# Kernel tuning notes

Hardware: AMD Instinct MI355X
Metric: run time of the kernel (lower is better)

The kernel has to match this reference:

```python
import jax, jax.numpy as jnp
import numpy as np

B, T, C, H = 4, 2048, 1024, 16
D = C // H  # head_dim = 64

def setup_inputs() -> dict:
    key = jax.random.key(0)
    ks = jax.random.split(key, 5)
    s = 0.02
    return {
        "x": jax.random.normal(ks[0], (B, T, C), dtype=jnp.float32),
        "W_attn": jax.random.normal(ks[1], (C, 3 * C), dtype=jnp.float32) * s,
        "b_attn": jnp.zeros((3 * C,), dtype=jnp.float32),
        "W_proj": jax.random.normal(ks[2], (C, C), dtype=jnp.float32) * s,
        "b_proj": jnp.zeros((C,), dtype=jnp.float32),
    }

def reference(x, W_attn, b_attn, W_proj, b_proj):
    Bx, Tx, Cx = x.shape
    qkv = x @ W_attn + b_attn                       # [B,T,3C]
    q, k, v = jnp.split(qkv, 3, axis=-1)
    def heads(t):
        return t.reshape(Bx, Tx, H, D).transpose(0, 2, 1, 3)  # [B,H,T,D]
    Q, K, V = heads(q), heads(k), heads(v)
    scale = 1.0 / np.sqrt(D).astype(np.float32)
    att = jnp.einsum('bhqd,bhkd->bhqk', Q, K) * scale        # [B,H,T,T]
    causal = jnp.tril(jnp.ones((Tx, Tx), dtype=bool))
    att = jnp.where(causal[None, None], att, -jnp.inf)
    att = jax.nn.softmax(att, axis=-1)
    y = jnp.einsum('bhqk,bhkd->bhqd', att, V)                # [B,H,T,D]
    y = y.transpose(0, 2, 1, 3).reshape(Bx, Tx, Cx)
    return y @ W_proj + b_proj
```

## Files before the change

### kernel.cpp

```cpp
#include <hip/hip_runtime.h>
#include <hip/hip_bf16.h>

#define B_ 4
#define T_ 2048
#define C_ 1024
#define H_ 16
#define D_ 64

using u16x4 = __attribute__((ext_vector_type(4))) unsigned short;
using u16x8 = __attribute__((ext_vector_type(8))) unsigned short;
using s16x8 = __attribute__((ext_vector_type(8))) short;
using f32x4v = __attribute__((ext_vector_type(4))) float;
using f32x16 = __attribute__((ext_vector_type(16))) float;

__device__ inline float bf2f(unsigned short u) {
  return __uint_as_float(((unsigned int)u) << 16);
}
__device__ inline unsigned short f2bf(float f) {
  unsigned int x = __float_as_uint(f);
  unsigned int r = (x + 0x7fffu + ((x >> 16) & 1u)) >> 16;
  return (unsigned short)r;
}
__device__ inline float fexp2(float x) {
  float r;
  asm("v_exp_f32 %0, %1" : "=v"(r) : "v"(x));
  return r;
}

__device__ inline unsigned cvtpk_bf16(float lo, float hi) {
  unsigned r;
  asm("v_cvt_pk_bf16_f32 %0, %1, %2" : "=v"(r) : "v"(lo), "v"(hi));
  return r;
}

__device__ inline s16x8 repack8(float p0, float p1, float p2, float p3,
                                float p4, float p5, float p6, float p7) {
  unsigned w0 = cvtpk_bf16(p0, p1), w1 = cvtpk_bf16(p2, p3);
  unsigned w2 = cvtpk_bf16(p4, p5), w3 = cvtpk_bf16(p6, p7);
  asm volatile("v_permlane32_swap_b32 %0, %1" : "+v"(w0), "+v"(w2));
  asm volatile("v_permlane32_swap_b32 %0, %1" : "+v"(w1), "+v"(w3));
  union { unsigned u[4]; s16x8 v; } r;
  r.u[0] = w0; r.u[1] = w1; r.u[2] = w2; r.u[3] = w3;
  return r.v;
}

__global__ __launch_bounds__(256) void cast_f32_bf16(const float* __restrict__ in,
                                                     ushort* __restrict__ out, int n4) {
  const int stride = gridDim.x * blockDim.x;
  for (int i = blockIdx.x * blockDim.x + threadIdx.x; i < n4; i += stride) {
    float4 v = ((const float4*)in)[i];
    u16x4 o = {f2bf(v.x), f2bf(v.y), f2bf(v.z), f2bf(v.w)};
    ((u16x4*)out)[i] = o;
  }
}

__global__ __launch_bounds__(256) void transpose_cast(const float* __restrict__ W,
                                                      ushort* __restrict__ Wt, int K, int N) {
  __shared__ float tile[64][65];
  const int n0 = blockIdx.x * 64, k0 = blockIdx.y * 64;
  const int tid = threadIdx.x;
  const int tr = tid >> 4, tc4 = (tid & 15) * 4;
#pragma unroll
  for (int i = 0; i < 4; ++i) {
    int r = tr + i * 16;
    float4 v = *(const float4*)&W[(size_t)(k0 + r) * N + n0 + tc4];
    tile[r][tc4 + 0] = v.x; tile[r][tc4 + 1] = v.y;
    tile[r][tc4 + 2] = v.z; tile[r][tc4 + 3] = v.w;
  }
  __syncthreads();
#pragma unroll
  for (int i = 0; i < 4; ++i) {
    int n = tr + i * 16;
    u16x4 o;
#pragma unroll
    for (int j = 0; j < 4; ++j) o[j] = f2bf(tile[tc4 + j][n]);
    *(u16x4*)&Wt[(size_t)(n0 + n) * K + k0 + tc4] = o;
  }
}

template <int BF16OUT, int NT>
__global__ __launch_bounds__(256) void gemm_bt(const ushort* __restrict__ A,
                                               const ushort* __restrict__ Bt,
                                               const float* __restrict__ bias,
                                               void* __restrict__ Cout,
                                               int M, int N, int K) {
  constexpr int BM = 128, BN = 128, BK = 64;
  __shared__ ushort Alds[2][BM * BK];
  __shared__ ushort Blds[2][BN * BK];
  const int tid = threadIdx.x;
  const int lane = tid & 63;
  const int w = tid >> 6;
  const int wr = w >> 1, wc = w & 1;
  const int nlin = blockIdx.y * gridDim.x + blockIdx.x;
  const int cpx = (gridDim.x * gridDim.y) >> 3;
  const int swzb = (nlin & 7) * cpx + (nlin >> 3);
  const int m0 = (swzb / gridDim.x) * BM;
  const int njbase = swzb % gridDim.x;

  const int ra = w * 32 + (lane >> 3);
  const int ca = ((lane & 7) * 8) ^ ((lane >> 3) << 3);
  const int swzr = (lane & 15 & 7) << 3;
  const int ko8 = (lane >> 4) * 8;
  const int l15 = lane & 15;

#define GB_STAGE(KK, BUF)                                                              \
  {                                                                                    \
    _Pragma("unroll") for (int i = 0; i < 4; ++i) {                                    \
      const ushort* ga = A + (size_t)(m0 + ra + i * 8) * K + (KK) + ca;                \
      __builtin_amdgcn_global_load_lds(                                                \
          (const __attribute__((address_space(1))) void*)ga,                           \
          (__attribute__((address_space(3))) void*)&Alds[BUF][w * 2048 + i * 512], 16, \
          0, 0);                                                                       \
      const ushort* gb = Bt + (size_t)(n0 + ra + i * 8) * K + (KK) + ca;               \
      __builtin_amdgcn_global_load_lds(                                                \
          (const __attribute__((address_space(1))) void*)gb,                           \
          (__attribute__((address_space(3))) void*)&Blds[BUF][w * 2048 + i * 512], 16, \
          0, 0);                                                                       \
    }                                                                                  \
  }

  for (int tt = 0; tt < NT; ++tt) {
    const int n0 = (njbase + tt * gridDim.x) * BN;
    f32x4v acc[4][4] = {};

    GB_STAGE(0, 0);
    asm volatile("s_waitcnt vmcnt(0)" ::: "memory");
    __builtin_amdgcn_s_barrier();
    asm volatile("" ::: "memory");

    int cur = 0;
    for (int k0 = 0; k0 < K; k0 += BK) {
      if (k0 + BK < K) GB_STAGE(k0 + BK, cur ^ 1);
#pragma unroll
      for (int ks = 0; ks < 2; ++ks) {
        s16x8 af[4], bfr[4];
#pragma unroll
        for (int m = 0; m < 4; ++m)
          af[m] = *(const s16x8*)&Alds[cur][(wr * 64 + m * 16 + l15) * BK +
                                            ((ks * 32 + ko8) ^ swzr)];
#pragma unroll
        for (int n = 0; n < 4; ++n)
          bfr[n] = *(const s16x8*)&Blds[cur][(wc * 64 + n * 16 + l15) * BK +
                                             ((ks * 32 + ko8) ^ swzr)];
#pragma unroll
        for (int m = 0; m < 4; ++m)
#pragma unroll
          for (int n = 0; n < 4; ++n)
            acc[m][n] = __builtin_amdgcn_mfma_f32_16x16x32_bf16(af[m], bfr[n], acc[m][n], 0, 0, 0);
      }
      asm volatile("s_waitcnt vmcnt(0) lgkmcnt(0)" ::: "memory");
      __builtin_amdgcn_s_barrier();
      asm volatile("" ::: "memory");
      cur ^= 1;
    }

#pragma unroll
    for (int m = 0; m < 4; ++m) {
      const int rg = m0 + wr * 64 + m * 16 + ((lane >> 4) * 4);
#pragma unroll
      for (int n = 0; n < 4; ++n) {
        const int cg = n0 + wc * 64 + n * 16 + l15;
        const float bv = bias[cg];
#pragma unroll
        for (int r2 = 0; r2 < 4; ++r2) {
          float v = acc[m][n][r2] + bv;
          if constexpr (BF16OUT)
            ((ushort*)Cout)[(size_t)(rg + r2) * N + cg] = f2bf(v);
          else
            ((float*)Cout)[(size_t)(rg + r2) * N + cg] = v;
        }
      }
    }
  }
#undef GB_STAGE
}

__global__ __launch_bounds__(256, 4) void attn_kernel(const ushort* __restrict__ qkv,
                                                      ushort* __restrict__ y) {
  constexpr int C3 = 3 * C_;
  const int n = blockIdx.x;
  const int c = n & 7;
  const int j = n >> 3;
  const int hbl = j & 7;
  const int qt = ((j >> 3) + hbl) & 15;
  const int hb = c * 8 + hbl;
  const int h = hb >> 2, b = hb & 3;
  const int tid = threadIdx.x;
  const int lane = tid & 63;
  const int w = tid >> 6;
  const int hi = lane >> 5;
  const int l31 = lane & 31;

  __shared__ __align__(16) ushort Klds[3][64 * 64];
  __shared__ __align__(16) ushort Vt[2][64 * 64];

  const int s_slot0 = (w * 2 + 0) * 1024 + lane * 16;
  const int s_slot1 = (w * 2 + 1) * 1024 + lane * 16;
  const int s_row0 = s_slot0 >> 7, s_row1 = s_slot1 >> 7;
  const int s_col0 = ((s_slot0 & 127) ^ ((s_row0 & 7) << 4)) >> 1;
  const int s_col1 = ((s_slot1 & 127) ^ ((s_row1 & 7) << 4)) >> 1;
  const ushort* kbase = qkv + (size_t)(b * T_) * C3 + C_ + h * D_;
  const ushort* vbase = qkv + (size_t)(b * T_) * C3 + 2 * C_ + h * D_;

  const int kv0 = l31 * 2;
  const int vdb = ((w << 1) | hi) * 8;

  s16x8 qf[4];
  {
    const ushort* qr = qkv + (size_t)(b * T_ + qt * 128 + w * 32 + l31) * C3 + h * D_;
#pragma unroll
    for (int ds = 0; ds < 4; ++ds) {
      s16x8 v = *(const s16x8*)(qr + ds * 16 + hi * 8);
#pragma unroll
      for (int jj = 0; jj < 8; ++jj)
        v[jj] = (short)f2bf(bf2f((unsigned short)v[jj]) * 0.18033688f);
      qf[ds] = v;
    }
  }

  const int ntile = 2 * qt + 2;
  const int nt_w = 2 * qt + 1 + (w >> 1);

  __builtin_amdgcn_global_load_lds(
      (const __attribute__((address_space(1))) void*)(kbase + (size_t)s_row0 * C3 + s_col0),
      (__attribute__((address_space(3))) void*)&Klds[0][(w * 2 + 0) * 512], 16, 0, 0);
  __builtin_amdgcn_global_load_lds(
      (const __attribute__((address_space(1))) void*)(kbase + (size_t)s_row1 * C3 + s_col1),
      (__attribute__((address_space(3))) void*)&Klds[0][(w * 2 + 1) * 512], 16, 0, 0);
  u16x8 vnA = *(const u16x8*)(vbase + (size_t)kv0 * C3 + vdb);
  u16x8 vnB = *(const u16x8*)(vbase + (size_t)(kv0 + 1) * C3 + vdb);
  if (ntile > 1) {
    __builtin_amdgcn_global_load_lds(
        (const __attribute__((address_space(1))) void*)(kbase + (size_t)(64 + s_row0) * C3 + s_col0),
        (__attribute__((address_space(3))) void*)&Klds[1][(w * 2 + 0) * 512], 16, 0, 0);
    __builtin_amdgcn_global_load_lds(
        (const __attribute__((address_space(1))) void*)(kbase + (size_t)(64 + s_row1) * C3 + s_col1),
        (__attribute__((address_space(3))) void*)&Klds[1][(w * 2 + 1) * 512], 16, 0, 0);
  }
#pragma unroll
  for (int jj = 0; jj < 8; ++jj) {
    int d = vdb + jj;
    *(unsigned*)&Vt[0][d * 64 + (kv0 ^ ((d & 7) << 3))] =
        (unsigned)vnA[jj] | ((unsigned)vnB[jj] << 16);
  }
  asm volatile("s_waitcnt lgkmcnt(0)" ::: "memory");
  __builtin_amdgcn_s_barrier();
  asm volatile("" ::: "memory");

  f32x16 yacc0 = {}, yacc1 = {};
  float lrun = 0.f;
  const int qg = qt * 128 + w * 32 + l31;

  int kcur = 0, vcur = 0;
  for (int t = 0; t < ntile; ++t) {
    const bool m1 = (t + 1 < ntile);
    const bool m2 = (t + 2 < ntile);
    if (m1) {
      const ushort* vrow = vbase + (size_t)((t + 1) * 64 + kv0) * C3;
      vnA = *(const u16x8*)(vrow + vdb);
      vnB = *(const u16x8*)(vrow + C3 + vdb);
    }
    if (m2) {
      const int kb2 = kcur >= 1 ? kcur - 1 : 2;
      __builtin_amdgcn_global_load_lds(
          (const __attribute__((address_space(1))) void*)(kbase + (size_t)((t + 2) * 64 + s_row0) * C3 + s_col0),
          (__attribute__((address_space(3))) void*)&Klds[kb2][(w * 2 + 0) * 512], 16, 0, 0);
      __builtin_amdgcn_global_load_lds(
          (const __attribute__((address_space(1))) void*)(kbase + (size_t)((t + 2) * 64 + s_row1) * C3 + s_col1),
          (__attribute__((address_space(3))) void*)&Klds[kb2][(w * 2 + 1) * 512], 16, 0, 0);
    }

    if (t < nt_w) {
      const bool diag = (t == nt_w - 1);
      const bool has_kb1 = (!diag) || ((w & 1) == 1);

      f32x16 sv0 = {}, sv1 = {};
      __builtin_amdgcn_s_setprio(1);
      {
        const int swr = (l31 & 7) << 3;
#pragma unroll
        for (int ds = 0; ds < 4; ++ds) {
          s16x8 kf = *(const s16x8*)&Klds[kcur][l31 * 64 + ((ds * 16 + hi * 8) ^ swr)];
          sv0 = __builtin_amdgcn_mfma_f32_32x32x16_bf16(kf, qf[ds], sv0, 0, 0, 0);
        }
      }
      if (has_kb1) {
        const int row = l31 + 32;
        const int swr = (row & 7) << 3;
#pragma unroll
        for (int ds = 0; ds < 4; ++ds) {
          s16x8 kf = *(const s16x8*)&Klds[kcur][row * 64 + ((ds * 16 + hi * 8) ^ swr)];
          sv1 = __builtin_amdgcn_mfma_f32_32x32x16_bf16(kf, qf[ds], sv1, 0, 0, 0);
        }
      }
      __builtin_amdgcn_s_setprio(0);

      if (diag) {
        const int kb0 = t * 64 + (w & 1) * 32 + 4 * hi;
        if ((w & 1) == 0) {
#pragma unroll
          for (int r = 0; r < 16; ++r)
            if (kb0 + (r & 3) + 8 * (r >> 2) > qg) sv0[r] = -1e30f;
        } else {
#pragma unroll
          for (int r = 0; r < 16; ++r)
            if (kb0 + (r & 3) + 8 * (r >> 2) > qg) sv1[r] = -1e30f;
        }
      }

      float l0_ = 0.f, l1_ = 0.f, l2_ = 0.f, l3_ = 0.f;
#pragma unroll
      for (int r = 0; r < 16; r += 4) {
        float p0v = fexp2(sv0[r]), p1v = fexp2(sv0[r + 1]);
        float p2v = fexp2(sv0[r + 2]), p3v = fexp2(sv0[r + 3]);
        sv0[r] = p0v; sv0[r + 1] = p1v; sv0[r + 2] = p2v; sv0[r + 3] = p3v;
        l0_ += p0v; l1_ += p1v; l2_ += p2v; l3_ += p3v;
      }
      if (has_kb1) {
#pragma unroll
        for (int r = 0; r < 16; r += 4) {
          float p0v = fexp2(sv1[r]), p1v = fexp2(sv1[r + 1]);
          float p2v = fexp2(sv1[r + 2]), p3v = fexp2(sv1[r + 3]);
          sv1[r] = p0v; sv1[r + 1] = p1v; sv1[r + 2] = p2v; sv1[r + 3] = p3v;
          l0_ += p0v; l1_ += p1v; l2_ += p2v; l3_ += p3v;
        }
      }
      float ls = (l0_ + l1_) + (l2_ + l3_);
      ls += __shfl_xor(ls, 32);
      lrun += ls;

      s16x8 pa0 = repack8(sv0[0], sv0[1], sv0[2], sv0[3], sv0[4], sv0[5], sv0[6], sv0[7]);
      s16x8 pa1 = repack8(sv0[8], sv0[9], sv0[10], sv0[11], sv0[12], sv0[13], sv0[14], sv0[15]);
      s16x8 pa2 = {}, pa3 = {};
      if (has_kb1) {
        pa2 = repack8(sv1[0], sv1[1], sv1[2], sv1[3], sv1[4], sv1[5], sv1[6], sv1[7]);
        pa3 = repack8(sv1[8], sv1[9], sv1[10], sv1[11], sv1[12], sv1[13], sv1[14], sv1[15]);
      }

      __builtin_amdgcn_s_setprio(1);
#pragma unroll
      for (int db = 0; db < 2; ++db) {
        const int d = db * 32 + l31;
        const int swz = (d & 7) << 3;
        s16x8 vf0 = *(const s16x8*)&Vt[vcur][d * 64 + ((0 + hi * 8) ^ swz)];
        s16x8 vf1 = *(const s16x8*)&Vt[vcur][d * 64 + ((16 + hi * 8) ^ swz)];
        if (db == 0) {
          yacc0 = __builtin_amdgcn_mfma_f32_32x32x16_bf16(vf0, pa0, yacc0, 0, 0, 0);
          yacc0 = __builtin_amdgcn_mfma_f32_32x32x16_bf16(vf1, pa1, yacc0, 0, 0, 0);
        } else {
          yacc1 = __builtin_amdgcn_mfma_f32_32x32x16_bf16(vf0, pa0, yacc1, 0, 0, 0);
          yacc1 = __builtin_amdgcn_mfma_f32_32x32x16_bf16(vf1, pa1, yacc1, 0, 0, 0);
        }
        if (has_kb1) {
          s16x8 vf2 = *(const s16x8*)&Vt[vcur][d * 64 + ((32 + hi * 8) ^ swz)];
          s16x8 vf3 = *(const s16x8*)&Vt[vcur][d * 64 + ((48 + hi * 8) ^ swz)];
          if (db == 0) {
            yacc0 = __builtin_amdgcn_mfma_f32_32x32x16_bf16(vf2, pa2, yacc0, 0, 0, 0);
            yacc0 = __builtin_amdgcn_mfma_f32_32x32x16_bf16(vf3, pa3, yacc0, 0, 0, 0);
          } else {
            yacc1 = __builtin_amdgcn_mfma_f32_32x32x16_bf16(vf2, pa2, yacc1, 0, 0, 0);
            yacc1 = __builtin_amdgcn_mfma_f32_32x32x16_bf16(vf3, pa3, yacc1, 0, 0, 0);
          }
        }
      }
      __builtin_amdgcn_s_setprio(0);
    }

    if (m1) {
#pragma unroll
      for (int jj = 0; jj < 8; ++jj) {
        int d = vdb + jj;
        *(unsigned*)&Vt[vcur ^ 1][d * 64 + (kv0 ^ ((d & 7) << 3))] =
            (unsigned)vnA[jj] | ((unsigned)vnB[jj] << 16);
      }
    }
    asm volatile("s_waitcnt lgkmcnt(0)" ::: "memory");
    __builtin_amdgcn_s_barrier();
    asm volatile("" ::: "memory");
    kcur = kcur == 2 ? 0 : kcur + 1;
    vcur ^= 1;
  }

  {
    const float inv = 1.f / lrun;
    yacc0 = yacc0 * inv;
    yacc1 = yacc1 * inv;
    ushort* tile = ((ushort*)Klds) + w * 2048;
    const int swq = (l31 & 7) << 3;
#pragma unroll
    for (int q4 = 0; q4 < 4; ++q4) {
      u16x4 p0, p1;
#pragma unroll
      for (int i = 0; i < 4; ++i) {
        p0[i] = f2bf(yacc0[q4 * 4 + i]);
        p1[i] = f2bf(yacc1[q4 * 4 + i]);
      }
      const int db0 = 8 * q4 + 4 * hi;
      *(u16x4*)&tile[l31 * 64 + (db0 ^ swq)] = p0;
      *(u16x4*)&tile[l31 * 64 + ((db0 + 32) ^ swq)] = p1;
    }
    const int eq = lane >> 1;
    const int ecb = (lane & 1) * 32;
    const int esz = (eq & 7) << 3;
    ushort* dst = y + (size_t)(b * T_ + qt * 128 + w * 32 + eq) * C_ + h * D_ + ecb;
#pragma unroll
    for (int cc = 0; cc < 4; ++cc) {
      u16x8 v = *(const u16x8*)&tile[eq * 64 + ((ecb + cc * 8) ^ esz)];
      *(u16x8*)(dst + cc * 8) = v;
    }
  }
}

extern "C" void kernel_launch(void* const* d_in, const int* in_sizes, int n_in,
                              void* d_out, int out_size, void* d_ws, size_t ws_size,
                              hipStream_t stream) {
  const float* x = (const float*)d_in[0];
  const float* W_attn = (const float*)d_in[1];
  const float* b_attn = (const float*)d_in[2];
  const float* W_proj = (const float*)d_in[3];
  const float* b_proj = (const float*)d_in[4];
  float* out = (float*)d_out;

  char* ws = (char*)d_ws;
  ushort* xb   = (ushort*)(ws);
  ushort* Wta  = (ushort*)(ws + (size_t)16777216);
  ushort* Wtp  = (ushort*)(ws + (size_t)23068672);
  ushort* qkvb = (ushort*)(ws + (size_t)25165824);
  ushort* yb   = (ushort*)(ws + (size_t)75497472);

  cast_f32_bf16<<<2048, 256, 0, stream>>>(x, xb, (B_ * T_ * C_) / 4);
  transpose_cast<<<dim3(48, 16), 256, 0, stream>>>(W_attn, Wta, C_, 3 * C_);
  transpose_cast<<<dim3(16, 16), 256, 0, stream>>>(W_proj, Wtp, C_, C_);
  gemm_bt<1, 3><<<dim3(8, 64), 256, 0, stream>>>(xb, Wta, b_attn, (void*)qkvb,
                                                 B_ * T_, 3 * C_, C_);
  attn_kernel<<<dim3(1024), 256, 0, stream>>>(qkvb, yb);
  gemm_bt<0, 1><<<dim3(8, 64), 256, 0, stream>>>(yb, Wtp, b_proj, (void*)out,
                                                 B_ * T_, C_, C_);
}
```

Before: 173.2 us.

## Pair causal query tiles per block to balance work and share K/V loads

Each attention block now handles two query tiles, p and 15-p, so every block does the same amount of causal work. Each K/V tile loaded into LDS is reused by both query tiles. The grid halves to 512 blocks and launch bounds drop to 2 blocks per CU, since doubled accumulators and Q fragments raise register pressure. The cost is fewer resident waves and less parallelism, which could hurt latency hiding.

```diff
diff --git a/kernel.cpp b/kernel.cpp
--- a/kernel.cpp
+++ b/kernel.cpp
@@ -175,14 +175,15 @@
 #undef GB_STAGE
 }
 
-__global__ __launch_bounds__(256, 4) void attn_kernel(const ushort* __restrict__ qkv,
+__global__ __launch_bounds__(256, 2) void attn_kernel(const ushort* __restrict__ qkv,
                                                       ushort* __restrict__ y) {
   constexpr int C3 = 3 * C_;
   const int n = blockIdx.x;
   const int c = n & 7;
   const int j = n >> 3;
   const int hbl = j & 7;
-  const int qt = ((j >> 3) + hbl) & 15;
+  const int p = j >> 3;
+  const int qtA = p, qtB = 15 - p;
   const int hb = c * 8 + hbl;
   const int h = hb >> 2, b = hb & 3;
   const int tid = threadIdx.x;
@@ -205,21 +206,29 @@
   const int kv0 = l31 * 2;
   const int vdb = ((w << 1) | hi) * 8;
 
-  s16x8 qf[4];
+  s16x8 qfA[4], qfB[4];
   {
-    const ushort* qr = qkv + (size_t)(b * T_ + qt * 128 + w * 32 + l31) * C3 + h * D_;
+    const ushort* qrA = qkv + (size_t)(b * T_ + qtA * 128 + w * 32 + l31) * C3 + h * D_;
+    const ushort* qrB = qkv + (size_t)(b * T_ + qtB * 128 + w * 32 + l31) * C3 + h * D_;
 #pragma unroll
     for (int ds = 0; ds < 4; ++ds) {
-      s16x8 v = *(const s16x8*)(qr + ds * 16 + hi * 8);
-#pragma unroll
-      for (int jj = 0; jj < 8; ++jj)
-        v[jj] = (short)f2bf(bf2f((unsigned short)v[jj]) * 0.18033688f);
-      qf[ds] = v;
-    }
-  }
-
-  const int ntile = 2 * qt + 2;
-  const int nt_w = 2 * qt + 1 + (w >> 1);
+      s16x8 va = *(const s16x8*)(qrA + ds * 16 + hi * 8);
+      s16x8 vb = *(const s16x8*)(qrB + ds * 16 + hi * 8);
+#pragma unroll
+      for (int jj = 0; jj < 8; ++jj) {
+        va[jj] = (short)f2bf(bf2f((unsigned short)va[jj]) * 0.18033688f);
+        vb[jj] = (short)f2bf(bf2f((unsigned short)vb[jj]) * 0.18033688f);
+      }
+      qfA[ds] = va;
+      qfB[ds] = vb;
+    }
+  }
+
+  const int ntile = 2 * qtB + 2;
+  const int nt_wA = 2 * qtA + 1 + (w >> 1);
+  const int nt_wB = 2 * qtB + 1 + (w >> 1);
+  const int qgA = qtA * 128 + w * 32 + l31;
+  const int qgB = qtB * 128 + w * 32 + l31;
 
   __builtin_amdgcn_global_load_lds(
       (const __attribute__((address_space(1))) void*)(kbase + (size_t)s_row0 * C3 + s_col0),
@@ -247,9 +256,93 @@
   __builtin_amdgcn_s_barrier();
   asm volatile("" ::: "memory");
 
-  f32x16 yacc0 = {}, yacc1 = {};
-  float lrun = 0.f;
-  const int qg = qt * 128 + w * 32 + l31;
+  f32x16 yaccA0 = {}, yaccA1 = {}, yaccB0 = {}, yaccB1 = {};
+  float lrunA = 0.f, lrunB = 0.f;
+
+#define ATTN_STEP(QF, Y0, Y1, LRUN, QG, NTW)                                           \
+  {                                                                                    \
+    const bool diag = (t == (NTW) - 1);                                                \
+    const bool has_kb1 = (!diag) || ((w & 1) == 1);                                    \
+    f32x16 sv0 = {}, sv1 = {};                                                         \
+    __builtin_amdgcn_s_setprio(1);                                                     \
+    {                                                                                  \
+      const int swr = (l31 & 7) << 3;                                                  \
+      _Pragma("unroll") for (int ds = 0; ds < 4; ++ds) {                               \
+        s16x8 kf = *(const s16x8*)&Klds[kcur][l31 * 64 + ((ds * 16 + hi * 8) ^ swr)];  \
+        sv0 = __builtin_amdgcn_mfma_f32_32x32x16_bf16(kf, QF[ds], sv0, 0, 0, 0);       \
+      }                                                                                \
+    }                                                                                  \
+    if (has_kb1) {                                                                     \
+      const int row = l31 + 32;                                                        \
+      const int swr = (row & 7) << 3;                                                  \
+      _Pragma("unroll") for (int ds = 0; ds < 4; ++ds) {                               \
+        s16x8 kf = *(const s16x8*)&Klds[kcur][row * 64 + ((ds * 16 + hi * 8) ^ swr)];  \
+        sv1 = __builtin_amdgcn_mfma_f32_32x32x16_bf16(kf, QF[ds], sv1, 0, 0, 0);       \
+      }                                                                                \
+    }                                                                                  \
+    __builtin_amdgcn_s_setprio(0);                                                     \
+    if (diag) {                                                                        \
+      const int kb0 = t * 64 + (w & 1) * 32 + 4 * hi;                                  \
+      if ((w & 1) == 0) {                                                              \
+        _Pragma("unroll") for (int r = 0; r < 16; ++r)                                 \
+            if (kb0 + (r & 3) + 8 * (r >> 2) > (QG)) sv0[r] = -1e30f;                  \
+      } else {                                                                         \
+        _Pragma("unroll") for (int r = 0; r < 16; ++r)                                 \
+            if (kb0 + (r & 3) + 8 * (r >> 2) > (QG)) sv1[r] = -1e30f;                  \
+      }                                                                                \
+    }                                                                                  \
+    float l0_ = 0.f, l1_ = 0.f, l2_ = 0.f, l3_ = 0.f;                                  \
+    _Pragma("unroll") for (int r = 0; r < 16; r += 4) {                                \
+      float p0v = fexp2(sv0[r]), p1v = fexp2(sv0[r + 1]);                              \
+      float p2v = fexp2(sv0[r + 2]), p3v = fexp2(sv0[r + 3]);                          \
+      sv0[r] = p0v; sv0[r + 1] = p1v; sv0[r + 2] = p2v; sv0[r + 3] = p3v;              \
+      l0_ += p0v; l1_ += p1v; l2_ += p2v; l3_ += p3v;                                  \
+    }                                                                                  \
+    if (has_kb1) {                                                                     \
+      _Pragma("unroll") for (int r = 0; r < 16; r += 4) {                              \
+        float p0v = fexp2(sv1[r]), p1v = fexp2(sv1[r + 1]);                            \
+        float p2v = fexp2(sv1[r + 2]), p3v = fexp2(sv1[r + 3]);                        \
+        sv1[r] = p0v; sv1[r + 1] = p1v; sv1[r + 2] = p2v; sv1[r + 3] = p3v;            \
+        l0_ += p0v; l1_ += p1v; l2_ += p2v; l3_ += p3v;                                \
+      }                                                                                \
+    }                                                                                  \
+    float ls = (l0_ + l1_) + (l2_ + l3_);                                              \
+    ls += __shfl_xor(ls, 32);                                                          \
+    LRUN += ls;                                                                        \
+    s16x8 pa0 = repack8(sv0[0], sv0[1], sv0[2], sv0[3], sv0[4], sv0[5], sv0[6], sv0[7]);  \
+    s16x8 pa1 = repack8(sv0[8], sv0[9], sv0[10], sv0[11], sv0[12], sv0[13], sv0[14], sv0[15]); \
+    s16x8 pa2 = {}, pa3 = {};                                                          \
+    if (has_kb1) {                                                                     \
+      pa2 = repack8(sv1[0], sv1[1], sv1[2], sv1[3], sv1[4], sv1[5], sv1[6], sv1[7]);   \
+      pa3 = repack8(sv1[8], sv1[9], sv1[10], sv1[11], sv1[12], sv1[13], sv1[14], sv1[15]); \
+    }                                                                                  \
+    __builtin_amdgcn_s_setprio(1);                                                     \
+    _Pragma("unroll") for (int db = 0; db < 2; ++db) {                                 \
+      const int d = db * 32 + l31;                                                     \
+      const int swz = (d & 7) << 3;                                                    \
+      s16x8 vf0 = *(const s16x8*)&Vt[vcur][d * 64 + ((0 + hi * 8) ^ swz)];             \
+      s16x8 vf1 = *(const s16x8*)&Vt[vcur][d * 64 + ((16 + hi * 8) ^ swz)];            \
+      if (db == 0) {                                                                   \
+        Y0 = __builtin_amdgcn_mfma_f32_32x32x16_bf16(vf0, pa0, Y0, 0, 0, 0);           \
+        Y0 = __builtin_amdgcn_mfma_f32_32x32x16_bf16(vf1, pa1, Y0, 0, 0, 0);           \
+      } else {                                                                         \
+        Y1 = __builtin_amdgcn_mfma_f32_32x32x16_bf16(vf0, pa0, Y1, 0, 0, 0);           \
+        Y1 = __builtin_amdgcn_mfma_f32_32x32x16_bf16(vf1, pa1, Y1, 0, 0, 0);           \
+      }                                                                                \
+      if (has_kb1) {                                                                   \
+        s16x8 vf2 = *(const s16x8*)&Vt[vcur][d * 64 + ((32 + hi * 8) ^ swz)];          \
+        s16x8 vf3 = *(const s16x8*)&Vt[vcur][d * 64 + ((48 + hi * 8) ^ swz)];          \
+        if (db == 0) {                                                                 \
+          Y0 = __builtin_amdgcn_mfma_f32_32x32x16_bf16(vf2, pa2, Y0, 0, 0, 0);         \
+          Y0 = __builtin_amdgcn_mfma_f32_32x32x16_bf16(vf3, pa3, Y0, 0, 0, 0);         \
+        } else {                                                                       \
+          Y1 = __builtin_amdgcn_mfma_f32_32x32x16_bf16(vf2, pa2, Y1, 0, 0, 0);         \
+          Y1 = __builtin_amdgcn_mfma_f32_32x32x16_bf16(vf3, pa3, Y1, 0, 0, 0);         \
+        }                                                                              \
+      }                                                                                \
+    }                                                                                  \
+    __builtin_amdgcn_s_setprio(0);                                                     \
+  }
 
   int kcur = 0, vcur = 0;
   for (int t = 0; t < ntile; ++t) {
@@ -270,101 +363,8 @@
           (__attribute__((address_space(3))) void*)&Klds[kb2][(w * 2 + 1) * 512], 16, 0, 0);
     }
 
-    if (t < nt_w) {
-      const bool diag = (t == nt_w - 1);
-      const bool has_kb1 = (!diag) || ((w & 1) == 1);
-
-      f32x16 sv0 = {}, sv1 = {};
-      __builtin_amdgcn_s_setprio(1);
-      {
-        const int swr = (l31 & 7) << 3;
-#pragma unroll
-        for (int ds = 0; ds < 4; ++ds) {
-          s16x8 kf = *(const s16x8*)&Klds[kcur][l31 * 64 + ((ds * 16 + hi * 8) ^ swr)];
-          sv0 = __builtin_amdgcn_mfma_f32_32x32x16_bf16(kf, qf[ds], sv0, 0, 0, 0);
-        }
-      }
-      if (has_kb1) {
-        const int row = l31 + 32;
-        const int swr = (row & 7) << 3;
-#pragma unroll
-        for (int ds = 0; ds < 4; ++ds) {
-          s16x8 kf = *(const s16x8*)&Klds[kcur][row * 64 + ((ds * 16 + hi * 8) ^ swr)];
-          sv1 = __builtin_amdgcn_mfma_f32_32x32x16_bf16(kf, qf[ds], sv1, 0, 0, 0);
-        }
-      }
-      __builtin_amdgcn_s_setprio(0);
-
-      if (diag) {
-        const int kb0 = t * 64 + (w & 1) * 32 + 4 * hi;
-        if ((w & 1) == 0) {
-#pragma unroll
-          for (int r = 0; r < 16; ++r)
-            if (kb0 + (r & 3) + 8 * (r >> 2) > qg) sv0[r] = -1e30f;
-        } else {
-#pragma unroll
-          for (int r = 0; r < 16; ++r)
-            if (kb0 + (r & 3) + 8 * (r >> 2) > qg) sv1[r] = -1e30f;
-        }
-      }
-
-      float l0_ = 0.f, l1_ = 0.f, l2_ = 0.f, l3_ = 0.f;
-#pragma unroll
-      for (int r = 0; r < 16; r += 4) {
-        float p0v = fexp2(sv0[r]), p1v = fexp2(sv0[r + 1]);
-        float p2v = fexp2(sv0[r + 2]), p3v = fexp2(sv0[r + 3]);
-        sv0[r] = p0v; sv0[r + 1] = p1v; sv0[r + 2] = p2v; sv0[r + 3] = p3v;
-        l0_ += p0v; l1_ += p1v; l2_ += p2v; l3_ += p3v;
-      }
-      if (has_kb1) {
-#pragma unroll
-        for (int r = 0; r < 16; r += 4) {
-          float p0v = fexp2(sv1[r]), p1v = fexp2(sv1[r + 1]);
-          float p2v = fexp2(sv1[r + 2]), p3v = fexp2(sv1[r + 3]);
-          sv1[r] = p0v; sv1[r + 1] = p1v; sv1[r + 2] = p2v; sv1[r + 3] = p3v;
-          l0_ += p0v; l1_ += p1v; l2_ += p2v; l3_ += p3v;
-        }
-      }
-      float ls = (l0_ + l1_) + (l2_ + l3_);
-      ls += __shfl_xor(ls, 32);
-      lrun += ls;
-
-      s16x8 pa0 = repack8(sv0[0], sv0[1], sv0[2], sv0[3], sv0[4], sv0[5], sv0[6], sv0[7]);
-      s16x8 pa1 = repack8(sv0[8], sv0[9], sv0[10], sv0[11], sv0[12], sv0[13], sv0[14], sv0[15]);
-      s16x8 pa2 = {}, pa3 = {};
-      if (has_kb1) {
-        pa2 = repack8(sv1[0], sv1[1], sv1[2], sv1[3], sv1[4], sv1[5], sv1[6], sv1[7]);
-        pa3 = repack8(sv1[8], sv1[9], sv1[10], sv1[11], sv1[12], sv1[13], sv1[14], sv1[15]);
-      }
-
-      __builtin_amdgcn_s_setprio(1);
-#pragma unroll
-      for (int db = 0; db < 2; ++db) {
-        const int d = db * 32 + l31;
-        const int swz = (d & 7) << 3;
-        s16x8 vf0 = *(const s16x8*)&Vt[vcur][d * 64 + ((0 + hi * 8) ^ swz)];
-        s16x8 vf1 = *(const s16x8*)&Vt[vcur][d * 64 + ((16 + hi * 8) ^ swz)];
-        if (db == 0) {
-          yacc0 = __builtin_amdgcn_mfma_f32_32x32x16_bf16(vf0, pa0, yacc0, 0, 0, 0);
-          yacc0 = __builtin_amdgcn_mfma_f32_32x32x16_bf16(vf1, pa1, yacc0, 0, 0, 0);
-        } else {
-          yacc1 = __builtin_amdgcn_mfma_f32_32x32x16_bf16(vf0, pa0, yacc1, 0, 0, 0);
-          yacc1 = __builtin_amdgcn_mfma_f32_32x32x16_bf16(vf1, pa1, yacc1, 0, 0, 0);
-        }
-        if (has_kb1) {
-          s16x8 vf2 = *(const s16x8*)&Vt[vcur][d * 64 + ((32 + hi * 8) ^ swz)];
-          s16x8 vf3 = *(const s16x8*)&Vt[vcur][d * 64 + ((48 + hi * 8) ^ swz)];
-          if (db == 0) {
-            yacc0 = __builtin_amdgcn_mfma_f32_32x32x16_bf16(vf2, pa2, yacc0, 0, 0, 0);
-            yacc0 = __builtin_amdgcn_mfma_f32_32x32x16_bf16(vf3, pa3, yacc0, 0, 0, 0);
-          } else {
-            yacc1 = __builtin_amdgcn_mfma_f32_32x32x16_bf16(vf2, pa2, yacc1, 0, 0, 0);
-            yacc1 = __builtin_amdgcn_mfma_f32_32x32x16_bf16(vf3, pa3, yacc1, 0, 0, 0);
-          }
-        }
-      }
-      __builtin_amdgcn_s_setprio(0);
-    }
+    if (t < nt_wB) ATTN_STEP(qfB, yaccB0, yaccB1, lrunB, qgB, nt_wB);
+    if (t < nt_wA) ATTN_STEP(qfA, yaccA0, yaccA1, lrunA, qgA, nt_wA);
 
     if (m1) {
 #pragma unroll
@@ -380,33 +380,42 @@
     kcur = kcur == 2 ? 0 : kcur + 1;
     vcur ^= 1;
   }
+#undef ATTN_STEP
 
   {
-    const float inv = 1.f / lrun;
-    yacc0 = yacc0 * inv;
-    yacc1 = yacc1 * inv;
-    ushort* tile = ((ushort*)Klds) + w * 2048;
     const int swq = (l31 & 7) << 3;
-#pragma unroll
-    for (int q4 = 0; q4 < 4; ++q4) {
-      u16x4 p0, p1;
-#pragma unroll
-      for (int i = 0; i < 4; ++i) {
-        p0[i] = f2bf(yacc0[q4 * 4 + i]);
-        p1[i] = f2bf(yacc1[q4 * 4 + i]);
-      }
-      const int db0 = 8 * q4 + 4 * hi;
-      *(u16x4*)&tile[l31 * 64 + (db0 ^ swq)] = p0;
-      *(u16x4*)&tile[l31 * 64 + ((db0 + 32) ^ swq)] = p1;
-    }
     const int eq = lane >> 1;
     const int ecb = (lane & 1) * 32;
     const int esz = (eq & 7) << 3;
-    ushort* dst = y + (size_t)(b * T_ + qt * 128 + w * 32 + eq) * C_ + h * D_ + ecb;
+    ushort* tileA = ((ushort*)Klds) + w * 2048;
+    ushort* tileB = ((ushort*)Vt) + w * 2048;
+    const float invA = 1.f / lrunA, invB = 1.f / lrunB;
+    yaccA0 = yaccA0 * invA; yaccA1 = yaccA1 * invA;
+    yaccB0 = yaccB0 * invB; yaccB1 = yaccB1 * invB;
+#pragma unroll
+    for (int q4 = 0; q4 < 4; ++q4) {
+      u16x4 a0, a1, b0, b1;
+#pragma unroll
+      for (int i = 0; i < 4; ++i) {
+        a0[i] = f2bf(yaccA0[q4 * 4 + i]);
+        a1[i] = f2bf(yaccA1[q4 * 4 + i]);
+        b0[i] = f2bf(yaccB0[q4 * 4 + i]);
+        b1[i] = f2bf(yaccB1[q4 * 4 + i]);
+      }
+      const int db0 = 8 * q4 + 4 * hi;
+      *(u16x4*)&tileA[l31 * 64 + (db0 ^ swq)] = a0;
+      *(u16x4*)&tileA[l31 * 64 + ((db0 + 32) ^ swq)] = a1;
+      *(u16x4*)&tileB[l31 * 64 + (db0 ^ swq)] = b0;
+      *(u16x4*)&tileB[l31 * 64 + ((db0 + 32) ^ swq)] = b1;
+    }
+    ushort* dstA = y + (size_t)(b * T_ + qtA * 128 + w * 32 + eq) * C_ + h * D_ + ecb;
+    ushort* dstB = y + (size_t)(b * T_ + qtB * 128 + w * 32 + eq) * C_ + h * D_ + ecb;
 #pragma unroll
     for (int cc = 0; cc < 4; ++cc) {
-      u16x8 v = *(const u16x8*)&tile[eq * 64 + ((ecb + cc * 8) ^ esz)];
-      *(u16x8*)(dst + cc * 8) = v;
+      u16x8 va = *(const u16x8*)&tileA[eq * 64 + ((ecb + cc * 8) ^ esz)];
+      u16x8 vb = *(const u16x8*)&tileB[eq * 64 + ((ecb + cc * 8) ^ esz)];
+      *(u16x8*)(dstA + cc * 8) = va;
+      *(u16x8*)(dstB + cc * 8) = vb;
     }
   }
 }
@@ -433,7 +442,7 @@
   transpose_cast<<<dim3(16, 16), 256, 0, stream>>>(W_proj, Wtp, C_, C_);
   gemm_bt<1, 3><<<dim3(8, 64), 256, 0, stream>>>(xb, Wta, b_attn, (void*)qkvb,
                                                  B_ * T_, 3 * C_, C_);
-  attn_kernel<<<dim3(1024), 256, 0, stream>>>(qkvb, yb);
+  attn_kernel<<<dim3(512), 256, 0, stream>>>(qkvb, yb);
   gemm_bt<0, 1><<<dim3(8, 64), 256, 0, stream>>>(yb, Wtp, b_proj, (void*)out,
                                                  B_ * T_, C_, C_);
 }
```

After: 165.8 us. 1.04x faster.

## Enlarge attention blocks to 256 query rows sharing K/V tiles across 8 waves

Applied to the files above, without the earlier changes.

Each attention workgroup now covers 256 query rows with 8 waves instead of 128 rows with 4 waves. Each K/V tile staged in shared memory is therefore reused by twice as many waves, which halves global K/V traffic per query. Query blocks are assigned in a folded order (0..3 then 7..4) to balance causal work, and the staging indices are reworked so each thread loads one 16-byte chunk. In exchange, V is written to LDS with 16-bit scalar stores instead of packed 32-bit stores. The launch bound of 512 threads with a minimum of 4 blocks per CU may squeeze registers and cause spills, and there are half as many blocks with more idle waves near the causal diagonal.

```diff
diff --git a/kernel.cpp b/kernel.cpp
--- a/kernel.cpp
+++ b/kernel.cpp
@@ -175,14 +175,15 @@
 #undef GB_STAGE
 }
 
-__global__ __launch_bounds__(256, 4) void attn_kernel(const ushort* __restrict__ qkv,
+__global__ __launch_bounds__(512, 4) void attn_kernel(const ushort* __restrict__ qkv,
                                                       ushort* __restrict__ y) {
   constexpr int C3 = 3 * C_;
   const int n = blockIdx.x;
   const int c = n & 7;
   const int j = n >> 3;
   const int hbl = j & 7;
-  const int qt = ((j >> 3) + hbl) & 15;
+  const int u = j >> 3;
+  const int qb = (u < 4) ? u : 11 - u;
   const int hb = c * 8 + hbl;
   const int h = hb >> 2, b = hb & 3;
   const int tid = threadIdx.x;
@@ -191,23 +192,19 @@
   const int hi = lane >> 5;
   const int l31 = lane & 31;
 
-  __shared__ __align__(16) ushort Klds[3][64 * 64];
-  __shared__ __align__(16) ushort Vt[2][64 * 64];
-
-  const int s_slot0 = (w * 2 + 0) * 1024 + lane * 16;
-  const int s_slot1 = (w * 2 + 1) * 1024 + lane * 16;
-  const int s_row0 = s_slot0 >> 7, s_row1 = s_slot1 >> 7;
-  const int s_col0 = ((s_slot0 & 127) ^ ((s_row0 & 7) << 4)) >> 1;
-  const int s_col1 = ((s_slot1 & 127) ^ ((s_row1 & 7) << 4)) >> 1;
+  __shared__ __align__(16) ushort SH[5 * 4096];
+
+  const int s_row = tid >> 3;
+  const int s_col = (((tid & 7) * 16) ^ ((s_row & 7) << 4)) >> 1;
   const ushort* kbase = qkv + (size_t)(b * T_) * C3 + C_ + h * D_;
   const ushort* vbase = qkv + (size_t)(b * T_) * C3 + 2 * C_ + h * D_;
 
-  const int kv0 = l31 * 2;
-  const int vdb = ((w << 1) | hi) * 8;
+  const int kvr = tid >> 3;
+  const int vdb = (tid & 7) * 8;
 
   s16x8 qf[4];
   {
-    const ushort* qr = qkv + (size_t)(b * T_ + qt * 128 + w * 32 + l31) * C3 + h * D_;
+    const ushort* qr = qkv + (size_t)(b * T_ + qb * 256 + w * 32 + l31) * C3 + h * D_;
 #pragma unroll
     for (int ds = 0; ds < 4; ++ds) {
       s16x8 v = *(const s16x8*)(qr + ds * 16 + hi * 8);
@@ -218,30 +215,23 @@
     }
   }
 
-  const int ntile = 2 * qt + 2;
-  const int nt_w = 2 * qt + 1 + (w >> 1);
+  const int ntile = 4 * qb + 4;
+  const int nt_w = 4 * qb + (w >> 1) + 1;
+  const int qg = qb * 256 + w * 32 + l31;
 
   __builtin_amdgcn_global_load_lds(
-      (const __attribute__((address_space(1))) void*)(kbase + (size_t)s_row0 * C3 + s_col0),
-      (__attribute__((address_space(3))) void*)&Klds[0][(w * 2 + 0) * 512], 16, 0, 0);
-  __builtin_amdgcn_global_load_lds(
-      (const __attribute__((address_space(1))) void*)(kbase + (size_t)s_row1 * C3 + s_col1),
-      (__attribute__((address_space(3))) void*)&Klds[0][(w * 2 + 1) * 512], 16, 0, 0);
-  u16x8 vnA = *(const u16x8*)(vbase + (size_t)kv0 * C3 + vdb);
-  u16x8 vnB = *(const u16x8*)(vbase + (size_t)(kv0 + 1) * C3 + vdb);
+      (const __attribute__((address_space(1))) void*)(kbase + (size_t)s_row * C3 + s_col),
+      (__attribute__((address_space(3))) void*)&SH[tid * 8], 16, 0, 0);
+  u16x8 vn = *(const u16x8*)(vbase + (size_t)kvr * C3 + vdb);
   if (ntile > 1) {
     __builtin_amdgcn_global_load_lds(
-        (const __attribute__((address_space(1))) void*)(kbase + (size_t)(64 + s_row0) * C3 + s_col0),
-        (__attribute__((address_space(3))) void*)&Klds[1][(w * 2 + 0) * 512], 16, 0, 0);
-    __builtin_amdgcn_global_load_lds(
-        (const __attribute__((address_space(1))) void*)(kbase + (size_t)(64 + s_row1) * C3 + s_col1),
-        (__attribute__((address_space(3))) void*)&Klds[1][(w * 2 + 1) * 512], 16, 0, 0);
+        (const __attribute__((address_space(1))) void*)(kbase + (size_t)(64 + s_row) * C3 + s_col),
+        (__attribute__((address_space(3))) void*)&SH[4096 + tid * 8], 16, 0, 0);
   }
 #pragma unroll
   for (int jj = 0; jj < 8; ++jj) {
     int d = vdb + jj;
-    *(unsigned*)&Vt[0][d * 64 + (kv0 ^ ((d & 7) << 3))] =
-        (unsigned)vnA[jj] | ((unsigned)vnB[jj] << 16);
+    SH[3 * 4096 + d * 64 + (kvr ^ ((d & 7) << 3))] = vn[jj];
   }
   asm volatile("s_waitcnt lgkmcnt(0)" ::: "memory");
   __builtin_amdgcn_s_barrier();
@@ -249,28 +239,22 @@
 
   f32x16 yacc0 = {}, yacc1 = {};
   float lrun = 0.f;
-  const int qg = qt * 128 + w * 32 + l31;
 
   int kcur = 0, vcur = 0;
   for (int t = 0; t < ntile; ++t) {
     const bool m1 = (t + 1 < ntile);
     const bool m2 = (t + 2 < ntile);
-    if (m1) {
-      const ushort* vrow = vbase + (size_t)((t + 1) * 64 + kv0) * C3;
-      vnA = *(const u16x8*)(vrow + vdb);
-      vnB = *(const u16x8*)(vrow + C3 + vdb);
-    }
+    if (m1) vn = *(const u16x8*)(vbase + (size_t)((t + 1) * 64 + kvr) * C3 + vdb);
     if (m2) {
       const int kb2 = kcur >= 1 ? kcur - 1 : 2;
       __builtin_amdgcn_global_load_lds(
-          (const __attribute__((address_space(1))) void*)(kbase + (size_t)((t + 2) * 64 + s_row0) * C3 + s_col0),
-          (__attribute__((address_space(3))) void*)&Klds[kb2][(w * 2 + 0) * 512], 16, 0, 0);
-      __builtin_amdgcn_global_load_lds(
-          (const __attribute__((address_space(1))) void*)(kbase + (size_t)((t + 2) * 64 + s_row1) * C3 + s_col1),
-          (__attribute__((address_space(3))) void*)&Klds[kb2][(w * 2 + 1) * 512], 16, 0, 0);
+          (const __attribute__((address_space(1))) void*)(kbase + (size_t)((t + 2) * 64 + s_row) * C3 + s_col),
+          (__attribute__((address_space(3))) void*)&SH[kb2 * 4096 + tid * 8], 16, 0, 0);
     }
 
     if (t < nt_w) {
+      const ushort* Kl = &SH[kcur * 4096];
+      const ushort* Vl = &SH[(3 + vcur) * 4096];
       const bool diag = (t == nt_w - 1);
       const bool has_kb1 = (!diag) || ((w & 1) == 1);
 
@@ -280,7 +264,7 @@
         const int swr = (l31 & 7) << 3;
 #pragma unroll
         for (int ds = 0; ds < 4; ++ds) {
-          s16x8 kf = *(const s16x8*)&Klds[kcur][l31 * 64 + ((ds * 16 + hi * 8) ^ swr)];
+          s16x8 kf = *(const s16x8*)&Kl[l31 * 64 + ((ds * 16 + hi * 8) ^ swr)];
           sv0 = __builtin_amdgcn_mfma_f32_32x32x16_bf16(kf, qf[ds], sv0, 0, 0, 0);
         }
       }
@@ -289,7 +273,7 @@
         const int swr = (row & 7) << 3;
 #pragma unroll
         for (int ds = 0; ds < 4; ++ds) {
-          s16x8 kf = *(const s16x8*)&Klds[kcur][row * 64 + ((ds * 16 + hi * 8) ^ swr)];
+          s16x8 kf = *(const s16x8*)&Kl[row * 64 + ((ds * 16 + hi * 8) ^ swr)];
           sv1 = __builtin_amdgcn_mfma_f32_32x32x16_bf16(kf, qf[ds], sv1, 0, 0, 0);
         }
       }
@@ -342,8 +326,8 @@
       for (int db = 0; db < 2; ++db) {
         const int d = db * 32 + l31;
         const int swz = (d & 7) << 3;
-        s16x8 vf0 = *(const s16x8*)&Vt[vcur][d * 64 + ((0 + hi * 8) ^ swz)];
-        s16x8 vf1 = *(const s16x8*)&Vt[vcur][d * 64 + ((16 + hi * 8) ^ swz)];
+        s16x8 vf0 = *(const s16x8*)&Vl[d * 64 + ((0 + hi * 8) ^ swz)];
+        s16x8 vf1 = *(const s16x8*)&Vl[d * 64 + ((16 + hi * 8) ^ swz)];
         if (db == 0) {
           yacc0 = __builtin_amdgcn_mfma_f32_32x32x16_bf16(vf0, pa0, yacc0, 0, 0, 0);
           yacc0 = __builtin_amdgcn_mfma_f32_32x32x16_bf16(vf1, pa1, yacc0, 0, 0, 0);
@@ -352,8 +336,8 @@
           yacc1 = __builtin_amdgcn_mfma_f32_32x32x16_bf16(vf1, pa1, yacc1, 0, 0, 0);
         }
         if (has_kb1) {
-          s16x8 vf2 = *(const s16x8*)&Vt[vcur][d * 64 + ((32 + hi * 8) ^ swz)];
-          s16x8 vf3 = *(const s16x8*)&Vt[vcur][d * 64 + ((48 + hi * 8) ^ swz)];
+          s16x8 vf2 = *(const s16x8*)&Vl[d * 64 + ((32 + hi * 8) ^ swz)];
+          s16x8 vf3 = *(const s16x8*)&Vl[d * 64 + ((48 + hi * 8) ^ swz)];
           if (db == 0) {
             yacc0 = __builtin_amdgcn_mfma_f32_32x32x16_bf16(vf2, pa2, yacc0, 0, 0, 0);
             yacc0 = __builtin_amdgcn_mfma_f32_32x32x16_bf16(vf3, pa3, yacc0, 0, 0, 0);
@@ -367,11 +351,11 @@
     }
 
     if (m1) {
+      ushort* Vn = &SH[(3 + (vcur ^ 1)) * 4096];
 #pragma unroll
       for (int jj = 0; jj < 8; ++jj) {
         int d = vdb + jj;
-        *(unsigned*)&Vt[vcur ^ 1][d * 64 + (kv0 ^ ((d & 7) << 3))] =
-            (unsigned)vnA[jj] | ((unsigned)vnB[jj] << 16);
+        Vn[d * 64 + (kvr ^ ((d & 7) << 3))] = vn[jj];
       }
     }
     asm volatile("s_waitcnt lgkmcnt(0)" ::: "memory");
@@ -385,7 +369,7 @@
     const float inv = 1.f / lrun;
     yacc0 = yacc0 * inv;
     yacc1 = yacc1 * inv;
-    ushort* tile = ((ushort*)Klds) + w * 2048;
+    ushort* tile = SH + w * 2048;
     const int swq = (l31 & 7) << 3;
 #pragma unroll
     for (int q4 = 0; q4 < 4; ++q4) {
@@ -402,7 +386,7 @@
     const int eq = lane >> 1;
     const int ecb = (lane & 1) * 32;
     const int esz = (eq & 7) << 3;
-    ushort* dst = y + (size_t)(b * T_ + qt * 128 + w * 32 + eq) * C_ + h * D_ + ecb;
+    ushort* dst = y + (size_t)(b * T_ + qb * 256 + w * 32 + eq) * C_ + h * D_ + ecb;
 #pragma unroll
     for (int cc = 0; cc < 4; ++cc) {
       u16x8 v = *(const u16x8*)&tile[eq * 64 + ((ecb + cc * 8) ^ esz)];
@@ -433,7 +417,7 @@
   transpose_cast<<<dim3(16, 16), 256, 0, stream>>>(W_proj, Wtp, C_, C_);
   gemm_bt<1, 3><<<dim3(8, 64), 256, 0, stream>>>(xb, Wta, b_attn, (void*)qkvb,
                                                  B_ * T_, 3 * C_, C_);
-  attn_kernel<<<dim3(1024), 256, 0, stream>>>(qkvb, yb);
+  attn_kernel<<<dim3(512), 512, 0, stream>>>(qkvb, yb);
   gemm_bt<0, 1><<<dim3(8, 64), 256, 0, stream>>>(yb, Wtp, b_proj, (void*)out,
                                                  B_ * T_, C_, C_);
 }
```

New measurement: 166.8 us. -3.7%, faster.
